# Kernel optimization log

Hardware: AMD Instinct MI355X
Metric: run time of the kernel (lower is better)

## Reference

```python
import jax, jax.numpy as jnp
import numpy as np
from jax import lax

SEQ_LEN = 15
LATENT = 16
HIDDEN = 64
OUT = 1
BATCH = 65536


def setup_inputs() -> dict:
    key = jax.random.key(0)
    ks = jax.random.split(key, 11)
    s = lambda *shape: 1.0 / np.sqrt(HIDDEN)
    def u(k, shape):
        return jax.random.uniform(k, shape, jnp.float32, -1.0 / np.sqrt(HIDDEN), 1.0 / np.sqrt(HIDDEN))
    return {
        "z": jax.random.normal(ks[0], (BATCH, LATENT), jnp.float32),
        "Wih0": u(ks[1], (4 * HIDDEN, LATENT)),
        "Whh0": u(ks[2], (4 * HIDDEN, HIDDEN)),
        "bih0": u(ks[3], (4 * HIDDEN,)),
        "bhh0": u(ks[4], (4 * HIDDEN,)),
        "Wih1": u(ks[5], (4 * HIDDEN, HIDDEN)),
        "Whh1": u(ks[6], (4 * HIDDEN, HIDDEN)),
        "bih1": u(ks[7], (4 * HIDDEN,)),
        "bhh1": u(ks[8], (4 * HIDDEN,)),
        "Wfc": u(ks[9], (OUT, HIDDEN)),
        "bfc": u(ks[10], (OUT,)),
    }


def lstm_layer(x, Wih, Whh, bih, bhh):
    # x: [B, T, D]. PyTorch gate order: i, f, g, o.
    B, T, _ = x.shape
    H = Whh.shape[1]
    # precompute input projections for all timesteps: [T, B, 4H]
    x_proj = jnp.einsum('btd,gd->tbg', x, Wih) + (bih + bhh)

    def step(carry, xp):
        h, c = carry
        gates = xp + h @ Whh.T
        i, f, g, o = jnp.split(gates, 4, axis=-1)
        i = jax.nn.sigmoid(i)
        f = jax.nn.sigmoid(f)
        g = jnp.tanh(g)
        o = jax.nn.sigmoid(o)
        c = f * c + i * g
        h = o * jnp.tanh(c)
        return (h, c), h

    h0 = jnp.zeros((B, H), x.dtype)
    _, ys = lax.scan(step, (h0, h0), x_proj)  # ys: [T, B, H]
    return jnp.swapaxes(ys, 0, 1)  # [B, T, H]


def reference(z, Wih0, Whh0, bih0, bhh0, Wih1, Whh1, bih1, bhh1, Wfc, bfc):
    # z: [B, latent] -> repeat along time: [B, T, latent]
    x = jnp.broadcast_to(z[:, None, :], (z.shape[0], SEQ_LEN, z.shape[1]))
    h1 = lstm_layer(x, Wih0, Whh0, bih0, bhh0)
    # (inter-layer dropout is inactive in eval mode)
    h2 = lstm_layer(h1, Wih1, Whh1, bih1, bhh1)
    return h2 @ Wfc.T + bfc  # [B, T, OUT]
```

## Files before the change

### kernel.cpp

```cpp
#include <hip/hip_runtime.h>

#define TSTEPS 15
#define HID    64
#define LAT    16
#define NBATCH 65536

typedef _Float16 v8h __attribute__((ext_vector_type(8)));
typedef _Float16 v4h __attribute__((ext_vector_type(4)));
typedef _Float16 v2h __attribute__((ext_vector_type(2)));
typedef float    v4f __attribute__((ext_vector_type(4)));

__device__ __forceinline__ float fast_sig(float x) {
    return __builtin_amdgcn_rcpf(1.0f + __expf(-x));
}
__device__ __forceinline__ float fast_tanh(float x) {
    return 2.0f * __builtin_amdgcn_rcpf(1.0f + __expf(-2.0f * x)) - 1.0f;
}

__device__ __forceinline__ v8h vzero8() {
    v8h v;
#pragma unroll
    for (int i = 0; i < 8; ++i) v[i] = (_Float16)0.0f;
    return v;
}

__device__ __forceinline__ v4h pack4(float a, float b, float c, float d) {
    const v2h lo = __builtin_bit_cast(v2h, __builtin_amdgcn_cvt_pkrtz(a, b));
    const v2h hi = __builtin_bit_cast(v2h, __builtin_amdgcn_cvt_pkrtz(c, d));
    return __builtin_shufflevector(lo, hi, 0, 1, 2, 3);
}

__global__ __launch_bounds__(512)
__attribute__((amdgpu_waves_per_eu(2, 2)))
void lstm2_pipe2(
        const float* __restrict__ z,
        const float* __restrict__ Wih0, const float* __restrict__ Whh0,
        const float* __restrict__ bih0, const float* __restrict__ bhh0,
        const float* __restrict__ Wih1, const float* __restrict__ Whh1,
        const float* __restrict__ bih1, const float* __restrict__ bhh1,
        const float* __restrict__ Wfc,  const float* __restrict__ bfc,
        float* __restrict__ out)
{
    __shared__ __align__(16) _Float16 wf[7 * 16 * 64 * 8];
    __shared__ __align__(16) _Float16 wfcf[2 * 64 * 8];
    __shared__ __align__(16) float    bsum1[256];
    __shared__ __align__(16) _Float16 state[8][32 * 72];

    const int tid  = threadIdx.x;
    const int wave = tid >> 6;
    const int lane = tid & 63;
    const int q    = lane >> 4;
    const int c    = lane & 15;
    const int row0 = blockIdx.x * 256 + wave * 32;

#pragma unroll 4
    for (int e = tid; e < 7 * 16 * 64 * 8; e += 512) {
        const int j  = e & 7;
        const int lm = (e >> 3) & 63;
        const int mt = (e >> 9) & 15;
        const int p  = e >> 13;
        const int g  = mt * 16 + (lm & 15);
        const int kk = (lm >> 4) * 8 + j;
        float v;
        if (p == 0)      v = (kk < LAT) ? Wih0[g * LAT + kk]
                           : (kk == LAT ? bih0[g] + bhh0[g] : 0.0f);
        else if (p == 1) v = Whh0[g * HID + kk];
        else if (p == 2) v = Whh0[g * HID + 32 + kk];
        else if (p == 3) v = Wih1[g * HID + kk];
        else if (p == 4) v = Wih1[g * HID + 32 + kk];
        else if (p == 5) v = Whh1[g * HID + kk];
        else             v = Whh1[g * HID + 32 + kk];
        wf[e] = (_Float16)v;
    }
#pragma unroll
    for (int e = tid; e < 2 * 64 * 8; e += 512) {
        const int j  = e & 7;
        const int lm = (e >> 3) & 63;
        const int kc = e >> 9;
        const int kk = kc * 32 + (lm >> 4) * 8 + j;
        wfcf[e] = ((lm & 15) == 0) ? (_Float16)Wfc[kk] : (_Float16)0.0f;
    }
    if (tid < 256) bsum1[tid] = bih1[tid] + bhh1[tid];
    __syncthreads();

    _Float16* stW = &state[wave][0];
    const float bfcv = bfc[0];

    v8h zfrag[2];
#pragma unroll
    for (int n = 0; n < 2; ++n) {
        zfrag[n] = vzero8();
        if (q < 2) {
            const float* zp = z + (size_t)(row0 + 16 * n + c) * LAT + q * 8;
            const float4 za = *(const float4*)(zp);
            const float4 zb = *(const float4*)(zp + 4);
            zfrag[n][0] = (_Float16)za.x; zfrag[n][1] = (_Float16)za.y;
            zfrag[n][2] = (_Float16)za.z; zfrag[n][3] = (_Float16)za.w;
            zfrag[n][4] = (_Float16)zb.x; zfrag[n][5] = (_Float16)zb.y;
            zfrag[n][6] = (_Float16)zb.z; zfrag[n][7] = (_Float16)zb.w;
        }
        if (q == 2) zfrag[n][0] = (_Float16)1.0f;
    }

    v8h hf[2][2], gf[2][2];
    v4h h1pk[4][2];
    float c0s[2][16], c1s[2][16];
#pragma unroll
    for (int n = 0; n < 2; ++n) {
        hf[n][0] = vzero8(); hf[n][1] = vzero8();
        gf[n][0] = vzero8(); gf[n][1] = vzero8();
#pragma unroll
        for (int i = 0; i < 16; ++i) { c0s[n][i] = 0.0f; c1s[n][i] = 0.0f; }
    }

#define AFRAG(pl, mt) (*(const v8h*)&wf[(((pl) * 16 + (mt)) * 64 + lane) * 8])
#define MFMA16(A, B, C) __builtin_amdgcn_mfma_f32_16x16x32_f16((A), (B), (C), 0, 0, 0)


    auto l0_part = [&]() {
#pragma unroll
        for (int a = 0; a < 4; ++a) {
            v4f acc0[2][4];
#pragma unroll
            for (int ty = 0; ty < 4; ++ty) {
                const int mt = 4 * ty + a;
                const v8h a0 = AFRAG(0, mt);
                const v8h a1 = AFRAG(1, mt);
                const v8h a2 = AFRAG(2, mt);
                v4f t0 = {0.f, 0.f, 0.f, 0.f};
                v4f t1 = {0.f, 0.f, 0.f, 0.f};
                t0 = MFMA16(a0, zfrag[0], t0);  t1 = MFMA16(a0, zfrag[1], t1);
                t0 = MFMA16(a1, hf[0][0], t0);  t1 = MFMA16(a1, hf[1][0], t1);
                t0 = MFMA16(a2, hf[0][1], t0);  t1 = MFMA16(a2, hf[1][1], t1);
                acc0[0][ty] = t0;  acc0[1][ty] = t1;
            }
#pragma unroll
            for (int n = 0; n < 2; ++n) {
                float hh[4];
#pragma unroll
                for (int r = 0; r < 4; ++r) {
                    const float ig = fast_sig(acc0[n][0][r]);
                    const float fg = fast_sig(acc0[n][1][r]);
                    const float gg = fast_tanh(acc0[n][2][r]);
                    const float og = fast_sig(acc0[n][3][r]);
                    const float cc = fg * c0s[n][a * 4 + r] + ig * gg;
                    c0s[n][a * 4 + r] = cc;
                    hh[r] = og * fast_tanh(cc);
                }
                *(v4h*)&stW[(c + 16 * n) * 72 + 16 * a + 4 * q] =
                    pack4(hh[0], hh[1], hh[2], hh[3]);
            }
        }
    };

    auto l1_part = [&]() {
#pragma unroll
        for (int a = 0; a < 4; ++a) {
            v4f acc1[2][4];
#pragma unroll
            for (int ty = 0; ty < 4; ++ty) {
                const int mt = 4 * ty + a;
                const v4f b  = *(const v4f*)&bsum1[64 * ty + 16 * a + 4 * q];
                const v8h a3 = AFRAG(3, mt);
                const v8h a4 = AFRAG(4, mt);
                const v8h a5 = AFRAG(5, mt);
                const v8h a6 = AFRAG(6, mt);
                v4f t0 = MFMA16(a3, hf[0][0], b);
                v4f t1 = MFMA16(a3, hf[1][0], b);
                t0 = MFMA16(a4, hf[0][1], t0);  t1 = MFMA16(a4, hf[1][1], t1);
                t0 = MFMA16(a5, gf[0][0], t0);  t1 = MFMA16(a5, gf[1][0], t1);
                t0 = MFMA16(a6, gf[0][1], t0);  t1 = MFMA16(a6, gf[1][1], t1);
                acc1[0][ty] = t0;  acc1[1][ty] = t1;
            }
#pragma unroll
            for (int n = 0; n < 2; ++n) {
                float hh[4];
#pragma unroll
                for (int r = 0; r < 4; ++r) {
                    const float ig = fast_sig(acc1[n][0][r]);
                    const float fg = fast_sig(acc1[n][1][r]);
                    const float gg = fast_tanh(acc1[n][2][r]);
                    const float og = fast_sig(acc1[n][3][r]);
                    const float cc = fg * c1s[n][a * 4 + r] + ig * gg;
                    c1s[n][a * 4 + r] = cc;
                    hh[r] = og * fast_tanh(cc);
                }
                h1pk[a][n] = pack4(hh[0], hh[1], hh[2], hh[3]);
            }
        }
    };

    auto l0_finish = [&]() {
#pragma unroll
        for (int n = 0; n < 2; ++n) {
            hf[n][0] = *(const v8h*)&stW[(c + 16 * n) * 72 + 8 * q];
            hf[n][1] = *(const v8h*)&stW[(c + 16 * n) * 72 + 32 + 8 * q];
        }
    };

    auto l1_finish = [&](int trow) {
#pragma unroll
        for (int a = 0; a < 4; ++a)
#pragma unroll
            for (int n = 0; n < 2; ++n)
                *(v4h*)&stW[(c + 16 * n) * 72 + 16 * a + 4 * q] = h1pk[a][n];
#pragma unroll
        for (int n = 0; n < 2; ++n) {
            gf[n][0] = *(const v8h*)&stW[(c + 16 * n) * 72 + 8 * q];
            gf[n][1] = *(const v8h*)&stW[(c + 16 * n) * 72 + 32 + 8 * q];
        }
        const v8h w0 = *(const v8h*)&wfcf[(0 * 64 + lane) * 8];
        const v8h w1 = *(const v8h*)&wfcf[(1 * 64 + lane) * 8];
#pragma unroll
        for (int n = 0; n < 2; ++n) {
            v4f f = {0.f, 0.f, 0.f, 0.f};
            f = MFMA16(w0, gf[n][0], f);
            f = MFMA16(w1, gf[n][1], f);
            if (lane < 16)
                out[(size_t)(row0 + 16 * n + lane) * TSTEPS + trow] = f[0] + bfcv;
        }
    };

    l0_part();
    l0_finish();

#pragma unroll 1
    for (int tt = 1; tt < TSTEPS; ++tt) {
        __asm__ __volatile__("" ::: "memory");
        l0_part();
        l1_part();
        l0_finish();
        l1_finish(tt - 1);
    }

    __asm__ __volatile__("" ::: "memory");
    l1_part();
    l1_finish(TSTEPS - 1);

#undef AFRAG
#undef MFMA16
}

extern "C" void kernel_launch(void* const* d_in, const int* in_sizes, int n_in,
                              void* d_out, int out_size, void* d_ws, size_t ws_size,
                              hipStream_t stream)
{
    (void)in_sizes; (void)n_in; (void)out_size; (void)d_ws; (void)ws_size;

    const float* z    = (const float*)d_in[0];
    const float* Wih0 = (const float*)d_in[1];
    const float* Whh0 = (const float*)d_in[2];
    const float* bih0 = (const float*)d_in[3];
    const float* bhh0 = (const float*)d_in[4];
    const float* Wih1 = (const float*)d_in[5];
    const float* Whh1 = (const float*)d_in[6];
    const float* bih1 = (const float*)d_in[7];
    const float* bhh1 = (const float*)d_in[8];
    const float* Wfc  = (const float*)d_in[9];
    const float* bfc  = (const float*)d_in[10];

    lstm2_pipe2<<<dim3(NBATCH / 256), dim3(512), 0, stream>>>(
        z, Wih0, Whh0, bih0, bhh0, Wih1, Whh1, bih1, bhh1, Wfc, bfc,
        (float*)d_out);
}
```

Before: 271.8 us.

## Precompute constant z-projection once and fold log2e into weights for cheaper gates

Layer 0's input z is the same at every timestep, so its projection (plus bias) is computed once with MFMA into registers and used as the accumulator init. This removes one MFMA pair per tile per step and one weight plane from LDS. The log2(e) factor is folded into the weights and biases so gates can use raw exp2. The sigmoid and tanh products are merged to share reciprocals, working on two lanes of float2 at a time. The step loop is reordered to run layer 1 before layer 0, which removes the h1 register staging, and the FC weights are hoisted out of the loop. The trade-off is more register pressure from holding 32 v4f z-projections per thread.

Result: faster. 254.8 us (-6.3%).

```diff
diff --git a/kernel.cpp b/kernel.cpp
--- a/kernel.cpp
+++ b/kernel.cpp
@@ -4,18 +4,13 @@
 #define HID    64
 #define LAT    16
 #define NBATCH 65536
+#define LOG2E  1.44269504088896f
 
 typedef _Float16 v8h __attribute__((ext_vector_type(8)));
 typedef _Float16 v4h __attribute__((ext_vector_type(4)));
 typedef _Float16 v2h __attribute__((ext_vector_type(2)));
 typedef float    v4f __attribute__((ext_vector_type(4)));
-
-__device__ __forceinline__ float fast_sig(float x) {
-    return __builtin_amdgcn_rcpf(1.0f + __expf(-x));
-}
-__device__ __forceinline__ float fast_tanh(float x) {
-    return 2.0f * __builtin_amdgcn_rcpf(1.0f + __expf(-2.0f * x)) - 1.0f;
-}
+typedef float    v2f __attribute__((ext_vector_type(2)));
 
 __device__ __forceinline__ v8h vzero8() {
     v8h v;
@@ -30,9 +25,33 @@
     return __builtin_shufflevector(lo, hi, 0, 1, 2, 3);
 }
 
+__device__ __forceinline__ v2f exp2_2(v2f x) {
+    v2f r; r.x = __builtin_amdgcn_exp2f(x.x); r.y = __builtin_amdgcn_exp2f(x.y);
+    return r;
+}
+__device__ __forceinline__ v2f rcp_2(v2f x) {
+    v2f r; r.x = __builtin_amdgcn_rcpf(x.x); r.y = __builtin_amdgcn_rcpf(x.y);
+    return r;
+}
+
+__device__ __forceinline__ v2f cell_update2(v2f ai, v2f af, v2f ag, v2f ao,
+                                            v2f& cst) {
+    const v2f one = {1.0f, 1.0f};
+    const v2f ei = exp2_2(-ai);
+    const v2f ef = exp2_2(-af);
+    const v2f eg = exp2_2(-2.0f * ag);
+    const v2f eo = exp2_2(-ao);
+    const v2f ig = (one - eg) * rcp_2((one + ei) * (one + eg));
+    const v2f f  = rcp_2(one + ef);
+    const v2f cc = f * cst + ig;
+    cst = cc;
+    const v2f ec = exp2_2(cc * (-2.0f * LOG2E));
+    return (one - ec) * rcp_2((one + eo) * (one + ec));
+}
+
 __global__ __launch_bounds__(512)
 __attribute__((amdgpu_waves_per_eu(2, 2)))
-void lstm2_pipe2(
+void lstm2_zp(
         const float* __restrict__ z,
         const float* __restrict__ Wih0, const float* __restrict__ Whh0,
         const float* __restrict__ bih0, const float* __restrict__ bhh0,
@@ -41,7 +60,7 @@
         const float* __restrict__ Wfc,  const float* __restrict__ bfc,
         float* __restrict__ out)
 {
-    __shared__ __align__(16) _Float16 wf[7 * 16 * 64 * 8];
+    __shared__ __align__(16) _Float16 wf[6 * 16 * 64 * 8];
     __shared__ __align__(16) _Float16 wfcf[2 * 64 * 8];
     __shared__ __align__(16) float    bsum1[256];
     __shared__ __align__(16) _Float16 state[8][32 * 72];
@@ -54,7 +73,7 @@
     const int row0 = blockIdx.x * 256 + wave * 32;
 
 #pragma unroll 4
-    for (int e = tid; e < 7 * 16 * 64 * 8; e += 512) {
+    for (int e = tid; e < 6 * 16 * 64 * 8; e += 512) {
         const int j  = e & 7;
         const int lm = (e >> 3) & 63;
         const int mt = (e >> 9) & 15;
@@ -62,15 +81,26 @@
         const int g  = mt * 16 + (lm & 15);
         const int kk = (lm >> 4) * 8 + j;
         float v;
-        if (p == 0)      v = (kk < LAT) ? Wih0[g * LAT + kk]
-                           : (kk == LAT ? bih0[g] + bhh0[g] : 0.0f);
-        else if (p == 1) v = Whh0[g * HID + kk];
-        else if (p == 2) v = Whh0[g * HID + 32 + kk];
-        else if (p == 3) v = Wih1[g * HID + kk];
-        else if (p == 4) v = Wih1[g * HID + 32 + kk];
-        else if (p == 5) v = Whh1[g * HID + kk];
+        if (p == 0)      v = Whh0[g * HID + kk];
+        else if (p == 1) v = Whh0[g * HID + 32 + kk];
+        else if (p == 2) v = Wih1[g * HID + kk];
+        else if (p == 3) v = Wih1[g * HID + 32 + kk];
+        else if (p == 4) v = Whh1[g * HID + kk];
         else             v = Whh1[g * HID + 32 + kk];
-        wf[e] = (_Float16)v;
+        wf[e] = (_Float16)(v * LOG2E);
+    }
+    _Float16* zw = &state[0][0];
+#pragma unroll 4
+    for (int e = tid; e < 16 * 64 * 8; e += 512) {
+        const int j  = e & 7;
+        const int lm = (e >> 3) & 63;
+        const int mt = e >> 9;
+        const int g  = mt * 16 + (lm & 15);
+        const int kk = (lm >> 4) * 8 + j;
+        float v = 0.0f;
+        if (kk < LAT)       v = Wih0[g * LAT + kk];
+        else if (kk == LAT) v = bih0[g] + bhh0[g];
+        zw[e] = (_Float16)(v * LOG2E);
     }
 #pragma unroll
     for (int e = tid; e < 2 * 64 * 8; e += 512) {
@@ -80,142 +110,143 @@
         const int kk = kc * 32 + (lm >> 4) * 8 + j;
         wfcf[e] = ((lm & 15) == 0) ? (_Float16)Wfc[kk] : (_Float16)0.0f;
     }
-    if (tid < 256) bsum1[tid] = bih1[tid] + bhh1[tid];
+    if (tid < 256) bsum1[tid] = (bih1[tid] + bhh1[tid]) * LOG2E;
     __syncthreads();
 
     _Float16* stW = &state[wave][0];
     const float bfcv = bfc[0];
 
-    v8h zfrag[2];
-#pragma unroll
-    for (int n = 0; n < 2; ++n) {
-        zfrag[n] = vzero8();
-        if (q < 2) {
-            const float* zp = z + (size_t)(row0 + 16 * n + c) * LAT + q * 8;
-            const float4 za = *(const float4*)(zp);
-            const float4 zb = *(const float4*)(zp + 4);
-            zfrag[n][0] = (_Float16)za.x; zfrag[n][1] = (_Float16)za.y;
-            zfrag[n][2] = (_Float16)za.z; zfrag[n][3] = (_Float16)za.w;
-            zfrag[n][4] = (_Float16)zb.x; zfrag[n][5] = (_Float16)zb.y;
-            zfrag[n][6] = (_Float16)zb.z; zfrag[n][7] = (_Float16)zb.w;
-        }
-        if (q == 2) zfrag[n][0] = (_Float16)1.0f;
-    }
+    const v8h wfc0 = *(const v8h*)&wfcf[(0 * 64 + lane) * 8];
+    const v8h wfc1 = *(const v8h*)&wfcf[(1 * 64 + lane) * 8];
+
+#define MFMA16(A, B, C) __builtin_amdgcn_mfma_f32_16x16x32_f16((A), (B), (C), 0, 0, 0)
+#define AFRAG(pl, mt) (*(const v8h*)&wf[(((pl) * 16 + (mt)) * 64 + lane) * 8])
+
+    v4f zproj[2][4][4];
+    {
+        v8h zfrag[2];
+#pragma unroll
+        for (int n = 0; n < 2; ++n) {
+            zfrag[n] = vzero8();
+            if (q < 2) {
+                const float* zp = z + (size_t)(row0 + 16 * n + c) * LAT + q * 8;
+                const float4 za = *(const float4*)(zp);
+                const float4 zb = *(const float4*)(zp + 4);
+                zfrag[n][0] = (_Float16)za.x; zfrag[n][1] = (_Float16)za.y;
+                zfrag[n][2] = (_Float16)za.z; zfrag[n][3] = (_Float16)za.w;
+                zfrag[n][4] = (_Float16)zb.x; zfrag[n][5] = (_Float16)zb.y;
+                zfrag[n][6] = (_Float16)zb.z; zfrag[n][7] = (_Float16)zb.w;
+            }
+            if (q == 2) zfrag[n][0] = (_Float16)1.0f;
+        }
+#pragma unroll
+        for (int a = 0; a < 4; ++a)
+#pragma unroll
+            for (int ty = 0; ty < 4; ++ty) {
+                const int mt = 4 * ty + a;
+                const v8h zwf = *(const v8h*)&zw[((size_t)mt * 64 + lane) * 8];
+                const v4f zz = {0.f, 0.f, 0.f, 0.f};
+                zproj[0][a][ty] = MFMA16(zwf, zfrag[0], zz);
+                zproj[1][a][ty] = MFMA16(zwf, zfrag[1], zz);
+            }
+    }
+    __syncthreads();
 
     v8h hf[2][2], gf[2][2];
-    v4h h1pk[4][2];
-    float c0s[2][16], c1s[2][16];
+    v2f c0s[2][8], c1s[2][8];
 #pragma unroll
     for (int n = 0; n < 2; ++n) {
         hf[n][0] = vzero8(); hf[n][1] = vzero8();
         gf[n][0] = vzero8(); gf[n][1] = vzero8();
 #pragma unroll
-        for (int i = 0; i < 16; ++i) { c0s[n][i] = 0.0f; c1s[n][i] = 0.0f; }
-    }
-
-#define AFRAG(pl, mt) (*(const v8h*)&wf[(((pl) * 16 + (mt)) * 64 + lane) * 8])
-#define MFMA16(A, B, C) __builtin_amdgcn_mfma_f32_16x16x32_f16((A), (B), (C), 0, 0, 0)
-
+        for (int i = 0; i < 8; ++i) { c0s[n][i] = (v2f){0.f, 0.f}; c1s[n][i] = (v2f){0.f, 0.f}; }
+    }
 
     auto l0_part = [&]() {
 #pragma unroll
         for (int a = 0; a < 4; ++a) {
-            v4f acc0[2][4];
+            v4f acc[2][4];
 #pragma unroll
             for (int ty = 0; ty < 4; ++ty) {
                 const int mt = 4 * ty + a;
                 const v8h a0 = AFRAG(0, mt);
                 const v8h a1 = AFRAG(1, mt);
-                const v8h a2 = AFRAG(2, mt);
-                v4f t0 = {0.f, 0.f, 0.f, 0.f};
-                v4f t1 = {0.f, 0.f, 0.f, 0.f};
-                t0 = MFMA16(a0, zfrag[0], t0);  t1 = MFMA16(a0, zfrag[1], t1);
-                t0 = MFMA16(a1, hf[0][0], t0);  t1 = MFMA16(a1, hf[1][0], t1);
-                t0 = MFMA16(a2, hf[0][1], t0);  t1 = MFMA16(a2, hf[1][1], t1);
-                acc0[0][ty] = t0;  acc0[1][ty] = t1;
+                v4f t0 = MFMA16(a0, hf[0][0], zproj[0][a][ty]);
+                v4f t1 = MFMA16(a0, hf[1][0], zproj[1][a][ty]);
+                t0 = MFMA16(a1, hf[0][1], t0);
+                t1 = MFMA16(a1, hf[1][1], t1);
+                acc[0][ty] = t0;  acc[1][ty] = t1;
             }
 #pragma unroll
             for (int n = 0; n < 2; ++n) {
-                float hh[4];
-#pragma unroll
-                for (int r = 0; r < 4; ++r) {
-                    const float ig = fast_sig(acc0[n][0][r]);
-                    const float fg = fast_sig(acc0[n][1][r]);
-                    const float gg = fast_tanh(acc0[n][2][r]);
-                    const float og = fast_sig(acc0[n][3][r]);
-                    const float cc = fg * c0s[n][a * 4 + r] + ig * gg;
-                    c0s[n][a * 4 + r] = cc;
-                    hh[r] = og * fast_tanh(cc);
-                }
+                const v2f h01 = cell_update2(
+                    (v2f){acc[n][0][0], acc[n][0][1]}, (v2f){acc[n][1][0], acc[n][1][1]},
+                    (v2f){acc[n][2][0], acc[n][2][1]}, (v2f){acc[n][3][0], acc[n][3][1]},
+                    c0s[n][a * 2]);
+                const v2f h23 = cell_update2(
+                    (v2f){acc[n][0][2], acc[n][0][3]}, (v2f){acc[n][1][2], acc[n][1][3]},
+                    (v2f){acc[n][2][2], acc[n][2][3]}, (v2f){acc[n][3][2], acc[n][3][3]},
+                    c0s[n][a * 2 + 1]);
                 *(v4h*)&stW[(c + 16 * n) * 72 + 16 * a + 4 * q] =
-                    pack4(hh[0], hh[1], hh[2], hh[3]);
-            }
+                    pack4(h01.x, h01.y, h23.x, h23.y);
+            }
+        }
+    };
+
+    auto l0_finish = [&]() {
+#pragma unroll
+        for (int n = 0; n < 2; ++n) {
+            hf[n][0] = *(const v8h*)&stW[(c + 16 * n) * 72 + 8 * q];
+            hf[n][1] = *(const v8h*)&stW[(c + 16 * n) * 72 + 32 + 8 * q];
         }
     };
 
     auto l1_part = [&]() {
 #pragma unroll
         for (int a = 0; a < 4; ++a) {
-            v4f acc1[2][4];
+            v4f acc[2][4];
 #pragma unroll
             for (int ty = 0; ty < 4; ++ty) {
                 const int mt = 4 * ty + a;
                 const v4f b  = *(const v4f*)&bsum1[64 * ty + 16 * a + 4 * q];
+                const v8h a2 = AFRAG(2, mt);
                 const v8h a3 = AFRAG(3, mt);
                 const v8h a4 = AFRAG(4, mt);
                 const v8h a5 = AFRAG(5, mt);
-                const v8h a6 = AFRAG(6, mt);
-                v4f t0 = MFMA16(a3, hf[0][0], b);
-                v4f t1 = MFMA16(a3, hf[1][0], b);
-                t0 = MFMA16(a4, hf[0][1], t0);  t1 = MFMA16(a4, hf[1][1], t1);
-                t0 = MFMA16(a5, gf[0][0], t0);  t1 = MFMA16(a5, gf[1][0], t1);
-                t0 = MFMA16(a6, gf[0][1], t0);  t1 = MFMA16(a6, gf[1][1], t1);
-                acc1[0][ty] = t0;  acc1[1][ty] = t1;
+                v4f t0 = MFMA16(a2, hf[0][0], b);
+                v4f t1 = MFMA16(a2, hf[1][0], b);
+                t0 = MFMA16(a3, hf[0][1], t0);  t1 = MFMA16(a3, hf[1][1], t1);
+                t0 = MFMA16(a4, gf[0][0], t0);  t1 = MFMA16(a4, gf[1][0], t1);
+                t0 = MFMA16(a5, gf[0][1], t0);  t1 = MFMA16(a5, gf[1][1], t1);
+                acc[0][ty] = t0;  acc[1][ty] = t1;
             }
 #pragma unroll
             for (int n = 0; n < 2; ++n) {
-                float hh[4];
-#pragma unroll
-                for (int r = 0; r < 4; ++r) {
-                    const float ig = fast_sig(acc1[n][0][r]);
-                    const float fg = fast_sig(acc1[n][1][r]);
-                    const float gg = fast_tanh(acc1[n][2][r]);
-                    const float og = fast_sig(acc1[n][3][r]);
-                    const float cc = fg * c1s[n][a * 4 + r] + ig * gg;
-                    c1s[n][a * 4 + r] = cc;
-                    hh[r] = og * fast_tanh(cc);
-                }
-                h1pk[a][n] = pack4(hh[0], hh[1], hh[2], hh[3]);
-            }
-        }
-    };
-
-    auto l0_finish = [&]() {
-#pragma unroll
-        for (int n = 0; n < 2; ++n) {
-            hf[n][0] = *(const v8h*)&stW[(c + 16 * n) * 72 + 8 * q];
-            hf[n][1] = *(const v8h*)&stW[(c + 16 * n) * 72 + 32 + 8 * q];
+                const v2f h01 = cell_update2(
+                    (v2f){acc[n][0][0], acc[n][0][1]}, (v2f){acc[n][1][0], acc[n][1][1]},
+                    (v2f){acc[n][2][0], acc[n][2][1]}, (v2f){acc[n][3][0], acc[n][3][1]},
+                    c1s[n][a * 2]);
+                const v2f h23 = cell_update2(
+                    (v2f){acc[n][0][2], acc[n][0][3]}, (v2f){acc[n][1][2], acc[n][1][3]},
+                    (v2f){acc[n][2][2], acc[n][2][3]}, (v2f){acc[n][3][2], acc[n][3][3]},
+                    c1s[n][a * 2 + 1]);
+                *(v4h*)&stW[(c + 16 * n) * 72 + 16 * a + 4 * q] =
+                    pack4(h01.x, h01.y, h23.x, h23.y);
+            }
         }
     };
 
     auto l1_finish = [&](int trow) {
-#pragma unroll
-        for (int a = 0; a < 4; ++a)
-#pragma unroll
-            for (int n = 0; n < 2; ++n)
-                *(v4h*)&stW[(c + 16 * n) * 72 + 16 * a + 4 * q] = h1pk[a][n];
 #pragma unroll
         for (int n = 0; n < 2; ++n) {
             gf[n][0] = *(const v8h*)&stW[(c + 16 * n) * 72 + 8 * q];
             gf[n][1] = *(const v8h*)&stW[(c + 16 * n) * 72 + 32 + 8 * q];
         }
-        const v8h w0 = *(const v8h*)&wfcf[(0 * 64 + lane) * 8];
-        const v8h w1 = *(const v8h*)&wfcf[(1 * 64 + lane) * 8];
 #pragma unroll
         for (int n = 0; n < 2; ++n) {
             v4f f = {0.f, 0.f, 0.f, 0.f};
-            f = MFMA16(w0, gf[n][0], f);
-            f = MFMA16(w1, gf[n][1], f);
+            f = MFMA16(wfc0, gf[n][0], f);
+            f = MFMA16(wfc1, gf[n][1], f);
             if (lane < 16)
                 out[(size_t)(row0 + 16 * n + lane) * TSTEPS + trow] = f[0] + bfcv;
         }
@@ -227,10 +258,10 @@
 #pragma unroll 1
     for (int tt = 1; tt < TSTEPS; ++tt) {
         __asm__ __volatile__("" ::: "memory");
+        l1_part();
+        l1_finish(tt - 1);
         l0_part();
-        l1_part();
         l0_finish();
-        l1_finish(tt - 1);
     }
 
     __asm__ __volatile__("" ::: "memory");
@@ -259,7 +290,7 @@
     const float* Wfc  = (const float*)d_in[9];
     const float* bfc  = (const float*)d_in[10];
 
-    lstm2_pipe2<<<dim3(NBATCH / 256), dim3(512), 0, stream>>>(
+    lstm2_zp<<<dim3(NBATCH / 256), dim3(512), 0, stream>>>(
         z, Wih0, Whh0, bih0, bhh0, Wih1, Whh1, bih1, bhh1, Wfc, bfc,
         (float*)d_out);
 }
```
